# Performance work log

Hardware: AMD Instinct MI355X
Metric: run time of the kernel (lower is better)

## Reference

```python
import jax, jax.numpy as jnp
import numpy as np

B, N, E, IN = 16, 4096, 65536, 128
FILTERS = [256, 256, 128]


def setup_inputs() -> dict:
    key = jax.random.key(0)
    ks = jax.random.split(key, 12)
    inp = {
        "x": jax.random.normal(ks[0], (B, N, IN), dtype=jnp.float32),
        "edge_index": jax.random.randint(ks[1], (B, 2, E), 0, N, dtype=jnp.int32),
        "edge_weight": jax.random.uniform(ks[2], (B, E), dtype=jnp.float32),
        "mask": jax.random.randint(ks[3], (B, N), 0, 2, dtype=jnp.int32),
    }
    dims = [IN] + FILTERS
    for i in range(3):
        inp[f"W{i+1}"] = jax.random.normal(ks[4 + 2 * i], (dims[i], dims[i + 1]), dtype=jnp.float32) / np.sqrt(dims[i]).astype(np.float32)
        inp[f"b{i+1}"] = 0.01 * jax.random.normal(ks[5 + 2 * i], (dims[i + 1],), dtype=jnp.float32)
    return inp


def _gcn_layer(x, ei, ew, valid, W, b):
    # GCNConv(add_self_loops=False, normalize=False):
    #   h = x @ W; out[v] = sum_{(u,v)} ew * h[u]; out += b (valid rows only)
    h = x @ W  # [N, d_out]
    u, v = ei[0], ei[1]
    evalid = valid[u] & valid[v]            # drop edges touching masked-out nodes
    w = jnp.where(evalid, ew, 0.0)
    agg = jnp.zeros_like(h).at[v].add(w[:, None] * h[u])
    return jnp.where(valid[:, None], agg + b, 0.0)


def reference(x, edge_index, edge_weight, mask, W1, b1, W2, b2, W3, b3):
    valid = mask > 0  # [B, N] bool
    out = x
    for W, b in ((W1, b1), (W2, b2), (W3, b3)):
        out = jax.vmap(_gcn_layer, in_axes=(0, 0, 0, 0, None, None))(
            out, edge_index, edge_weight, valid, W, b)
        out = jax.nn.relu(out)  # dropout p=0.0 -> identity
    return out
```

## Files before the change

kernel.cpp:

```cpp
#include <hip/hip_runtime.h>

static constexpr int BATCH = 16;
static constexpr int NNODE = 4096;
static constexpr int NEDGE = 65536;
static constexpr int ROWS  = BATCH * NNODE;
static constexpr int CAP   = 2432;
static constexpr int PM    = BATCH * CAP;

typedef _Float16 half8  __attribute__((ext_vector_type(8)));
typedef _Float16 half4v __attribute__((ext_vector_type(4)));
typedef _Float16 half2v __attribute__((ext_vector_type(2)));
typedef float    f32x4  __attribute__((ext_vector_type(4)));
typedef float    f32x2  __attribute__((ext_vector_type(2)));

#define GP(p) (const __attribute__((address_space(1))) void*)(p)
#define LP(p) (__attribute__((address_space(3))) void*)(p)


__global__ __launch_bounds__(256) void count_kernel(
    const int* __restrict__ ei, const int* __restrict__ mask,
    int* __restrict__ counts)
{
    const int idx = blockIdx.x * 256 + threadIdx.x;
    const int b = idx >> 16;
    const int e = idx & (NEDGE - 1);
    const int* eib = ei + (size_t)b * 2 * NEDGE;
    const int u = eib[e];
    const int v = eib[NEDGE + e];
    const int mrow = b * NNODE;
    if (mask[mrow + u] != 0 && mask[mrow + v] != 0)
        atomicAdd(&counts[mrow + v], 1);
}

__global__ __launch_bounds__(256) void scan_compact_kernel(
    const int* __restrict__ counts, const int* __restrict__ mask,
    int* __restrict__ row_start, int* __restrict__ cursor,
    int* __restrict__ vlist, int* __restrict__ cidx, int* __restrict__ validN)
{
    __shared__ int sums[256];
    const int b = blockIdx.x, t = threadIdx.x;

    const int* mb = mask + b * NNODE;
    for (int i = t; i < CAP; i += 256) vlist[b * CAP + i] = 0;

    int loc[16]; int s = 0;
    #pragma unroll
    for (int i = 0; i < 16; ++i) { loc[i] = (mb[t * 16 + i] != 0); s += loc[i]; }
    sums[t] = s;
    __syncthreads();
    for (int off = 1; off < 256; off <<= 1) {
        int v = (t >= off) ? sums[t - off] : 0;
        __syncthreads();
        sums[t] += v;
        __syncthreads();
    }
    int run = (t == 0) ? 0 : sums[t - 1];
    #pragma unroll
    for (int i = 0; i < 16; ++i) {
        const int n = t * 16 + i;
        if (loc[i]) {
            if (run < CAP) { vlist[b * CAP + run] = n; cidx[b * NNODE + n] = b * CAP + run; }
            ++run;
        } else {
            cidx[b * NNODE + n] = 0;
        }
    }
    if (t == 255) validN[b] = run;
    __syncthreads();

    const int* c = counts + b * NNODE;
    int* rs = row_start + b * (NNODE + 1);
    int* cu = cursor + b * NNODE;

    int local[16]; s = 0;
    #pragma unroll
    for (int i = 0; i < 16; ++i) { local[i] = c[t * 16 + i]; s += local[i]; }
    sums[t] = s;
    __syncthreads();
    for (int off = 1; off < 256; off <<= 1) {
        int v = (t >= off) ? sums[t - off] : 0;
        __syncthreads();
        sums[t] += v;
        __syncthreads();
    }
    run = (t == 0) ? 0 : sums[t - 1];
    #pragma unroll
    for (int i = 0; i < 16; ++i) { rs[t * 16 + i] = run; cu[t * 16 + i] = run; run += local[i]; }
    if (t == 255) rs[NNODE] = run;
}

__global__ __launch_bounds__(256) void fill_kernel(
    const int* __restrict__ ei, const float* __restrict__ ew,
    const int* __restrict__ mask, const int* __restrict__ cidx,
    int* __restrict__ cursor, unsigned int* __restrict__ bkt)
{
    const int idx = blockIdx.x * 256 + threadIdx.x;
    const int b = idx >> 16;
    const int e = idx & (NEDGE - 1);
    const int* eib = ei + (size_t)b * 2 * NEDGE;
    const int u = eib[e];
    const int v = eib[NEDGE + e];
    const int mrow = b * NNODE;
    if (mask[mrow + u] != 0 && mask[mrow + v] != 0) {
        const _Float16 w = (_Float16)ew[(size_t)b * NEDGE + e];
        const unsigned short wb = __builtin_bit_cast(unsigned short, w);
        const unsigned uc = (unsigned)cidx[mrow + u];
        const int pos = atomicAdd(&cursor[mrow + v], 1);
        bkt[(size_t)b * NEDGE + pos] = ((unsigned)wb << 16) | uc;
    }
}


__global__ __launch_bounds__(256) void prep_kernel(
    const float* __restrict__ X, const int* __restrict__ vlist,
    const float* __restrict__ W1, const float* __restrict__ W2,
    const float* __restrict__ W3,
    _Float16* __restrict__ X16c, _Float16* __restrict__ Wt1,
    _Float16* __restrict__ Wt2, _Float16* __restrict__ Wt3)
{
    const int idx = blockIdx.x * 256 + threadIdx.x;
    if (idx < PM * 32) {
        const int row = idx >> 5;
        const int c4  = idx & 31;
        const int b   = row / CAP;
        const int v   = vlist[row];
        const float4 s = *(const float4*)&X[((size_t)b * NNODE + v) * 128 + c4 * 4];
        half4v h = {(_Float16)s.x, (_Float16)s.y, (_Float16)s.z, (_Float16)s.w};
        *(half4v*)&X16c[(size_t)row * 128 + c4 * 4] = h;
    } else {
        const int i = idx - PM * 32;
        if (i < 32768) {
            int k = i >> 8, n = i & 255;
            Wt1[n * 128 + k] = (_Float16)W1[i];
        } else if (i < 98304) {
            int j = i - 32768;
            int k = j >> 8, n = j & 255;
            Wt2[n * 256 + k] = (_Float16)W2[j];
        } else {
            int j = i - 98304;
            int k = j >> 7, n = j & 127;
            Wt3[n * 256 + k] = (_Float16)W3[j];
        }
    }
}

template<int K, int N, bool EPI>
__global__ __launch_bounds__(256, 2) void gemm_full(
    const _Float16* __restrict__ Xc,
    const _Float16* __restrict__ Wt,
    const float* __restrict__ bias,
    _Float16* __restrict__ Hc)
{
    constexpr int NCH  = CAP / 128;
    constexpr int NPAN = K / 32;
    constexpr int NI   = N / 32;
    constexpr int CB   = N / 2;
    constexpr int RST  = CB + 8;
    __shared__ _Float16 A16[NPAN * 128 * 32];

    const int tid  = threadIdx.x;
    const int lane = tid & 63;
    const int wave = tid >> 6;
    const int wr = wave >> 1, wc = wave & 1;
    const int quad = lane >> 4;
    const int l15  = lane & 15;

    const int xcd  = blockIdx.x & 7;
    const int j    = blockIdx.x >> 3;
    const int batch = 2 * xcd + (j >= NCH);
    const int tile  = (j >= NCH) ? j - NCH : j;
    const size_t bm = (size_t)batch * CAP + (size_t)tile * 128;

    const int srow = tid >> 2;
    const int sch  = (tid & 3) * 8;
    #pragma unroll
    for (int pp = 0; pp < NPAN; ++pp)
        #pragma unroll
        for (int rnd = 0; rnd < 2; ++rnd)
            __builtin_amdgcn_global_load_lds(
                GP(Xc + (bm + rnd * 64 + srow) * K + pp * 32 + sch),
                LP(A16 + pp * 4096 + rnd * 2048 + tid * 8), 16, 0, 0);
    __syncthreads();

    f32x4 acc[4][NI];
    #pragma unroll
    for (int mi = 0; mi < 4; ++mi)
        #pragma unroll
        for (int ni = 0; ni < NI; ++ni) acc[mi][ni] = (f32x4)0.0f;

    const _Float16* ap = A16 + (wr * 64 + l15) * 32 + quad * 8;
    const _Float16* wp = Wt + (size_t)(wc * CB + l15) * K + quad * 8;

    #pragma unroll
    for (int pp = 0; pp < NPAN; ++pp) {
        half8 af[4], bf[NI];
        #pragma unroll
        for (int mi = 0; mi < 4; ++mi)
            af[mi] = *(const half8*)(ap + pp * 4096 + mi * 16 * 32);
        #pragma unroll
        for (int ni = 0; ni < NI; ++ni)
            bf[ni] = *(const half8*)(wp + (size_t)ni * 16 * K + pp * 32);
        #pragma unroll
        for (int mi = 0; mi < 4; ++mi)
            #pragma unroll
            for (int ni = 0; ni < NI; ++ni)
                acc[mi][ni] = __builtin_amdgcn_mfma_f32_16x16x32_f16(
                    bf[ni], af[mi], acc[mi][ni], 0, 0, 0);
    }
    __syncthreads();

    _Float16* stg = A16 + wave * 16 * RST;
    const int rr = lane >> 2;
    const int c0 = lane & 3;
    #pragma unroll
    for (int mi = 0; mi < 4; ++mi) {
        #pragma unroll
        for (int ni = 0; ni < NI; ++ni) {
            f32x4 v = acc[mi][ni];
            half4v o;
            if (EPI) {
                const f32x4 bv = *(const f32x4*)&bias[wc * CB + ni * 16 + quad * 4];
                #pragma unroll
                for (int r = 0; r < 4; ++r) o[r] = (_Float16)fmaxf(v[r] + bv[r], 0.0f);
            } else {
                #pragma unroll
                for (int r = 0; r < 4; ++r) o[r] = (_Float16)v[r];
            }
            *(half4v*)&stg[l15 * RST + ni * 16 + quad * 4] = o;
        }
        const size_t grow = bm + wr * 64 + mi * 16 + rr;
        _Float16* hp = &Hc[grow * N + wc * CB];
        #pragma unroll
        for (int c = 0; c < NI / 2; ++c) {
            const int ch = (c0 + 4 * c) * 8;
            half8 v = *(const half8*)&stg[rr * RST + ch];
            *(half8*)(hp + ch) = v;
        }
    }
}

__global__ __launch_bounds__(256, 2) void gemm23_kernel(
    const _Float16* __restrict__ Xc,
    const _Float16* __restrict__ Wt2,
    const _Float16* __restrict__ Wt3,
    const float* __restrict__ b2,
    _Float16* __restrict__ H3)
{
    constexpr int K    = 256;
    constexpr int NPAN = K / 32;
    constexpr int NCH  = CAP / 128;
    __shared__ _Float16 A16[NPAN * 128 * 32];

    const int tid  = threadIdx.x;
    const int lane = tid & 63;
    const int wave = tid >> 6;
    const int wr = wave >> 1, wc = wave & 1;
    const int quad = lane >> 4;
    const int l15  = lane & 15;

    const int xcd  = blockIdx.x & 7;
    const int j    = blockIdx.x >> 3;
    const int batch = 2 * xcd + (j >= NCH);
    const int tile  = (j >= NCH) ? j - NCH : j;
    const size_t bm = (size_t)batch * CAP + (size_t)tile * 128;

    const int srow = tid >> 2;
    const int sch  = (tid & 3) * 8;
    #pragma unroll
    for (int pp = 0; pp < NPAN; ++pp)
        #pragma unroll
        for (int rnd = 0; rnd < 2; ++rnd)
            __builtin_amdgcn_global_load_lds(
                GP(Xc + (bm + rnd * 64 + srow) * K + pp * 32 + sch),
                LP(A16 + pp * 4096 + rnd * 2048 + tid * 8), 16, 0, 0);
    __syncthreads();

    f32x4 acc[4][8];
    #pragma unroll
    for (int mi = 0; mi < 4; ++mi)
        #pragma unroll
        for (int ni = 0; ni < 8; ++ni) acc[mi][ni] = (f32x4)0.0f;

    const _Float16* ap = A16 + (wr * 64 + l15) * 32 + quad * 8;
    const _Float16* wp = Wt2 + (size_t)(wc * 128 + l15) * K + quad * 8;

    #pragma unroll
    for (int pp = 0; pp < NPAN; ++pp) {
        half8 af[4], bf[8];
        #pragma unroll
        for (int mi = 0; mi < 4; ++mi)
            af[mi] = *(const half8*)(ap + pp * 4096 + mi * 16 * 32);
        #pragma unroll
        for (int ni = 0; ni < 8; ++ni)
            bf[ni] = *(const half8*)(wp + (size_t)ni * 16 * K + pp * 32);
        #pragma unroll
        for (int mi = 0; mi < 4; ++mi)
            #pragma unroll
            for (int ni = 0; ni < 8; ++ni)
                acc[mi][ni] = __builtin_amdgcn_mfma_f32_16x16x32_f16(
                    bf[ni], af[mi], acc[mi][ni], 0, 0, 0);
    }
    __syncthreads();

    #pragma unroll
    for (int mi = 0; mi < 4; ++mi) {
        const int row = wr * 64 + mi * 16 + l15;
        #pragma unroll
        for (int ni = 0; ni < 8; ++ni) {
            const int col = wc * 128 + ni * 16 + quad * 4;
            const f32x4 bv = *(const f32x4*)&b2[col];
            f32x4 v = acc[mi][ni];
            half4v o;
            #pragma unroll
            for (int r = 0; r < 4; ++r) o[r] = (_Float16)fmaxf(v[r] + bv[r], 0.0f);
            *(half4v*)&A16[(col >> 5) * 4096 + row * 32 + (col & 31)] = o;
        }
    }
    __syncthreads();

    f32x4 acc2[4][4];
    #pragma unroll
    for (int mi = 0; mi < 4; ++mi)
        #pragma unroll
        for (int ni = 0; ni < 4; ++ni) acc2[mi][ni] = (f32x4)0.0f;

    const _Float16* wp3 = Wt3 + (size_t)(wc * 64 + l15) * K + quad * 8;
    #pragma unroll
    for (int pp = 0; pp < NPAN; ++pp) {
        half8 af[4], bf[4];
        #pragma unroll
        for (int mi = 0; mi < 4; ++mi)
            af[mi] = *(const half8*)(ap + pp * 4096 + mi * 16 * 32);
        #pragma unroll
        for (int ni = 0; ni < 4; ++ni)
            bf[ni] = *(const half8*)(wp3 + (size_t)ni * 16 * K + pp * 32);
        #pragma unroll
        for (int mi = 0; mi < 4; ++mi)
            #pragma unroll
            for (int ni = 0; ni < 4; ++ni)
                acc2[mi][ni] = __builtin_amdgcn_mfma_f32_16x16x32_f16(
                    bf[ni], af[mi], acc2[mi][ni], 0, 0, 0);
    }
    __syncthreads();

    constexpr int RST = 72;
    _Float16* stg = A16 + wave * 16 * RST;
    const int rr = lane >> 2;
    const int c0 = lane & 3;
    #pragma unroll
    for (int mi = 0; mi < 4; ++mi) {
        #pragma unroll
        for (int ni = 0; ni < 4; ++ni) {
            f32x4 v = acc2[mi][ni];
            half4v o;
            #pragma unroll
            for (int r = 0; r < 4; ++r) o[r] = (_Float16)v[r];
            *(half4v*)&stg[l15 * RST + ni * 16 + quad * 4] = o;
        }
        const size_t grow = bm + wr * 64 + mi * 16 + rr;
        _Float16* hp = &H3[grow * 128 + wc * 64];
        #pragma unroll
        for (int c = 0; c < 2; ++c) {
            const int ch = (c0 + 4 * c) * 8;
            half8 v = *(const half8*)&stg[rr * RST + ch];
            *(half8*)(hp + ch) = v;
        }
    }
}


__global__ __launch_bounds__(256) void gather_x(
    const int* __restrict__ row_start, const unsigned int* __restrict__ bkt,
    const _Float16* __restrict__ X,
    const int* __restrict__ vlist, const int* __restrict__ validN,
    _Float16* __restrict__ OUT)
{
    constexpr int NU = CAP / 4;
    const int tid  = threadIdx.x;
    const int lane = tid & 63;
    const int wave = tid >> 6;

    const int xcd  = blockIdx.x & 7;
    const int jj   = blockIdx.x >> 3;
    const int batch = 2 * xcd + (jj >= NU);
    const int unit  = (jj >= NU) ? jj - NU : jj;

    const int j = unit * 4 + wave;
    if (j >= validN[batch]) return;
    const int g = batch * CAP + j;
    const int v = vlist[g];

    const int* rs = row_start + batch * (NNODE + 1);
    const int s = rs[v], e = rs[v + 1];
    const unsigned* bk = bkt + (size_t)batch * NEDGE;
    const _Float16* Hb = X + lane * 2;

    float acc[2] = {};
    for (int i = s; i < e; i += 8) {
        const int cnt = e - i;
        unsigned pk[8];
        #pragma unroll
        for (int t = 0; t < 8; ++t) pk[t] = bk[i + t];
        const unsigned u0 = pk[0] & 0xffffu;
        float wj[8]; const _Float16* hp[8];
        #pragma unroll
        for (int t = 0; t < 8; ++t) {
            const bool ok = (t < cnt);
            const unsigned u = ok ? (pk[t] & 0xffffu) : u0;
            wj[t] = ok ? (float)__builtin_bit_cast(_Float16, (unsigned short)(pk[t] >> 16)) : 0.0f;
            hp[t] = Hb + (size_t)u * 128;
        }
        half2v hv[8];
        #pragma unroll
        for (int t = 0; t < 8; ++t) hv[t] = *(const half2v*)hp[t];
        #pragma unroll
        for (int t = 0; t < 8; ++t)
            #pragma unroll
            for (int c = 0; c < 2; ++c) acc[c] += wj[t] * (float)hv[t][c];
    }
    half2v o = {(_Float16)acc[0], (_Float16)acc[1]};
    *(half2v*)&OUT[(size_t)g * 128 + lane * 2] = o;
}

__global__ __launch_bounds__(256) void gather_agg(
    const int* __restrict__ row_start, const unsigned int* __restrict__ bkt,
    const _Float16* __restrict__ H,
    const int* __restrict__ vlist, const int* __restrict__ validN,
    _Float16* __restrict__ OUT)
{
    constexpr int NU = CAP / 4;
    const int tid  = threadIdx.x;
    const int lane = tid & 63;
    const int wave = tid >> 6;

    const int xcd  = blockIdx.x & 7;
    const int jj   = blockIdx.x >> 3;
    const int batch = 2 * xcd + (jj >= NU);
    const int unit  = (jj >= NU) ? jj - NU : jj;

    const int j = unit * 4 + wave;
    if (j >= validN[batch]) return;
    const int g = batch * CAP + j;
    const int v = vlist[g];

    const int* rs = row_start + batch * (NNODE + 1);
    const int s = rs[v], e = rs[v + 1];
    const unsigned* bk = bkt + (size_t)batch * NEDGE;
    const _Float16* Hb = H + lane * 4;

    float acc[4] = {};
    for (int i = s; i < e; i += 8) {
        const int cnt = e - i;
        unsigned pk[8];
        #pragma unroll
        for (int t = 0; t < 8; ++t) pk[t] = bk[i + t];
        const unsigned u0 = pk[0] & 0xffffu;
        float wj[8]; const _Float16* hp[8];
        #pragma unroll
        for (int t = 0; t < 8; ++t) {
            const bool ok = (t < cnt);
            const unsigned u = ok ? (pk[t] & 0xffffu) : u0;
            wj[t] = ok ? (float)__builtin_bit_cast(_Float16, (unsigned short)(pk[t] >> 16)) : 0.0f;
            hp[t] = Hb + (size_t)u * 256;
        }
        half4v hv[8];
        #pragma unroll
        for (int t = 0; t < 8; ++t) hv[t] = *(const half4v*)hp[t];
        #pragma unroll
        for (int t = 0; t < 8; ++t)
            #pragma unroll
            for (int c = 0; c < 4; ++c) acc[c] += wj[t] * (float)hv[t][c];
    }
    half4v o;
    #pragma unroll
    for (int c = 0; c < 4; ++c) o[c] = (_Float16)acc[c];
    *(half4v*)&OUT[(size_t)g * 256 + lane * 4] = o;
}

__global__ __launch_bounds__(256) void gather_final(
    const int* __restrict__ row_start, const unsigned int* __restrict__ bkt,
    const _Float16* __restrict__ H,
    const int* __restrict__ mask, const float* __restrict__ bias,
    float* __restrict__ OUT)
{
    constexpr int NU = NNODE / 4;
    const int tid  = threadIdx.x;
    const int lane = tid & 63;
    const int wave = tid >> 6;

    const int xcd  = blockIdx.x & 7;
    const int jj   = blockIdx.x >> 3;
    const int batch = 2 * xcd + (jj >= NU);
    const int unit  = (jj >= NU) ? jj - NU : jj;

    const int n = unit * 4 + wave;
    const int mrow = batch * NNODE + n;

    float acc[2] = {};
    if (mask[mrow] != 0) {
        const int* rs = row_start + batch * (NNODE + 1);
        const int s = rs[n], e = rs[n + 1];
        const unsigned* bk = bkt + (size_t)batch * NEDGE;
        const _Float16* Hb = H + lane * 2;

        for (int i = s; i < e; i += 8) {
            const int cnt = e - i;
            unsigned pk[8];
            #pragma unroll
            for (int t = 0; t < 8; ++t) pk[t] = bk[i + t];
            const unsigned u0 = pk[0] & 0xffffu;
            float wj[8]; const _Float16* hp[8];
            #pragma unroll
            for (int t = 0; t < 8; ++t) {
                const bool ok = (t < cnt);
                const unsigned u = ok ? (pk[t] & 0xffffu) : u0;
                wj[t] = ok ? (float)__builtin_bit_cast(_Float16, (unsigned short)(pk[t] >> 16)) : 0.0f;
                hp[t] = Hb + (size_t)u * 128;
            }
            half2v hv[8];
            #pragma unroll
            for (int t = 0; t < 8; ++t) hv[t] = *(const half2v*)hp[t];
            #pragma unroll
            for (int t = 0; t < 8; ++t)
                #pragma unroll
                for (int c = 0; c < 2; ++c) acc[c] += wj[t] * (float)hv[t][c];
        }
        #pragma unroll
        for (int c = 0; c < 2; ++c)
            acc[c] = fmaxf(acc[c] + bias[lane * 2 + c], 0.0f);
    }
    f32x2 o = {acc[0], acc[1]};
    *(f32x2*)&OUT[(size_t)mrow * 128 + lane * 2] = o;
}

extern "C" void kernel_launch(void* const* d_in, const int* in_sizes, int n_in,
                              void* d_out, int out_size, void* d_ws, size_t ws_size,
                              hipStream_t stream) {
    const float* x    = (const float*)d_in[0];
    const int*   ei   = (const int*)  d_in[1];
    const float* ew   = (const float*)d_in[2];
    const int*   mask = (const int*)  d_in[3];
    const float* W1   = (const float*)d_in[4];
    const float* b1   = (const float*)d_in[5];
    const float* W2   = (const float*)d_in[6];
    const float* b2   = (const float*)d_in[7];
    const float* W3   = (const float*)d_in[8];
    const float* b3   = (const float*)d_in[9];
    float* out = (float*)d_out;

    char* ws = (char*)d_ws;
    _Float16* X16c = (_Float16*)(ws);
    _Float16* AggX = (_Float16*)(ws + (10u << 20));
    _Float16* H3c  = AggX;
    _Float16* Ac   = (_Float16*)(ws + (20u << 20));
    _Float16* AggA = (_Float16*)(ws + (40u << 20));
    unsigned int* bkt = (unsigned int*)(ws + (60u << 20));
    _Float16* Wt1  = (_Float16*)(ws + (64u << 20));
    _Float16* Wt2  = Wt1 + 128 * 256;
    _Float16* Wt3  = Wt2 + 256 * 256;
    int* counts    = (int*)(Wt3 + 256 * 128);
    int* row_start = counts + ROWS;
    int* cursor    = row_start + BATCH * (NNODE + 1);
    int* cidx      = cursor + ROWS;
    int* vlist     = cidx + ROWS;
    int* validN    = vlist + PM;

    const dim3 blk(256);
    const int edgeBlocks = BATCH * NEDGE / 256;

    hipMemsetAsync(counts, 0, (size_t)ROWS * sizeof(int), stream);
    count_kernel<<<edgeBlocks, blk, 0, stream>>>(ei, mask, counts);
    scan_compact_kernel<<<BATCH, blk, 0, stream>>>(counts, mask, row_start, cursor,
                                                   vlist, cidx, validN);
    fill_kernel<<<edgeBlocks, blk, 0, stream>>>(ei, ew, mask, cidx, cursor, bkt);

    const int prepBlocks = (PM * 32 + 131072) / 256;
    prep_kernel<<<prepBlocks, blk, 0, stream>>>(x, vlist, W1, W2, W3,
                                                X16c, Wt1, Wt2, Wt3);

    const int gemmBlocks = PM / 128;
    const int midBlocks  = PM / 4;
    const int finBlocks  = ROWS / 4;

    gather_x<<<midBlocks, blk, 0, stream>>>(row_start, bkt, X16c, vlist, validN, AggX);
    gemm_full<128, 256, true><<<gemmBlocks, blk, 0, stream>>>(AggX, Wt1, b1, Ac);

    gather_agg<<<midBlocks, blk, 0, stream>>>(row_start, bkt, Ac, vlist, validN, AggA);
    gemm23_kernel<<<gemmBlocks, blk, 0, stream>>>(AggA, Wt2, Wt3, b2, H3c);

    gather_final<<<finBlocks, blk, 0, stream>>>(row_start, bkt, H3c, mask, b3, out);
}
```

Baseline: 242.6 us.

## Split scan into parallel blocks, fuse fill with prep, halve GEMM row tiles

The scan/compact kernel now runs mask compaction and count scan in separate blocks (2*BATCH blocks) instead of serially within one block. The edge-fill and X/weight prep kernels are merged into one launch, which removes a launch and lets both phases overlap. Both GEMM kernels move from 128-row to 64-row tiles, with each wave owning a column slice, and launch bounds rise to 3 blocks per CU. This doubles the grid and raises occupancy, at the cost of loading each weight column once per 64 rows instead of per 128.

```diff
diff --git a/kernel.cpp b/kernel.cpp
--- a/kernel.cpp
+++ b/kernel.cpp
@@ -38,130 +38,131 @@
     int* __restrict__ vlist, int* __restrict__ cidx, int* __restrict__ validN)
 {
     __shared__ int sums[256];
-    const int b = blockIdx.x, t = threadIdx.x;
-
-    const int* mb = mask + b * NNODE;
-    for (int i = t; i < CAP; i += 256) vlist[b * CAP + i] = 0;
-
-    int loc[16]; int s = 0;
-    #pragma unroll
-    for (int i = 0; i < 16; ++i) { loc[i] = (mb[t * 16 + i] != 0); s += loc[i]; }
-    sums[t] = s;
-    __syncthreads();
-    for (int off = 1; off < 256; off <<= 1) {
-        int v = (t >= off) ? sums[t - off] : 0;
+    const int t = threadIdx.x;
+
+    if (blockIdx.x < BATCH) {
+        const int b = blockIdx.x;
+        const int* c = counts + b * NNODE;
+        int* rs = row_start + b * (NNODE + 1);
+        int* cu = cursor + b * NNODE;
+
+        int local[16]; int s = 0;
+        #pragma unroll
+        for (int i = 0; i < 16; ++i) { local[i] = c[t * 16 + i]; s += local[i]; }
+        sums[t] = s;
         __syncthreads();
-        sums[t] += v;
+        for (int off = 1; off < 256; off <<= 1) {
+            int v = (t >= off) ? sums[t - off] : 0;
+            __syncthreads();
+            sums[t] += v;
+            __syncthreads();
+        }
+        int run = (t == 0) ? 0 : sums[t - 1];
+        #pragma unroll
+        for (int i = 0; i < 16; ++i) { rs[t * 16 + i] = run; cu[t * 16 + i] = run; run += local[i]; }
+        if (t == 255) rs[NNODE] = run;
+    } else {
+        const int b = blockIdx.x - BATCH;
+        const int* mb = mask + b * NNODE;
+        for (int i = t; i < CAP; i += 256) vlist[b * CAP + i] = 0;
+
+        int loc[16]; int s = 0;
+        #pragma unroll
+        for (int i = 0; i < 16; ++i) { loc[i] = (mb[t * 16 + i] != 0); s += loc[i]; }
+        sums[t] = s;
         __syncthreads();
-    }
-    int run = (t == 0) ? 0 : sums[t - 1];
-    #pragma unroll
-    for (int i = 0; i < 16; ++i) {
-        const int n = t * 16 + i;
-        if (loc[i]) {
-            if (run < CAP) { vlist[b * CAP + run] = n; cidx[b * NNODE + n] = b * CAP + run; }
-            ++run;
-        } else {
-            cidx[b * NNODE + n] = 0;
-        }
-    }
-    if (t == 255) validN[b] = run;
-    __syncthreads();
-
-    const int* c = counts + b * NNODE;
-    int* rs = row_start + b * (NNODE + 1);
-    int* cu = cursor + b * NNODE;
-
-    int local[16]; s = 0;
-    #pragma unroll
-    for (int i = 0; i < 16; ++i) { local[i] = c[t * 16 + i]; s += local[i]; }
-    sums[t] = s;
-    __syncthreads();
-    for (int off = 1; off < 256; off <<= 1) {
-        int v = (t >= off) ? sums[t - off] : 0;
-        __syncthreads();
-        sums[t] += v;
-        __syncthreads();
-    }
-    run = (t == 0) ? 0 : sums[t - 1];
-    #pragma unroll
-    for (int i = 0; i < 16; ++i) { rs[t * 16 + i] = run; cu[t * 16 + i] = run; run += local[i]; }
-    if (t == 255) rs[NNODE] = run;
-}
-
-__global__ __launch_bounds__(256) void fill_kernel(
+        for (int off = 1; off < 256; off <<= 1) {
+            int v = (t >= off) ? sums[t - off] : 0;
+            __syncthreads();
+            sums[t] += v;
+            __syncthreads();
+        }
+        int run = (t == 0) ? 0 : sums[t - 1];
+        #pragma unroll
+        for (int i = 0; i < 16; ++i) {
+            const int n = t * 16 + i;
+            if (loc[i]) {
+                if (run < CAP) { vlist[b * CAP + run] = n; cidx[b * NNODE + n] = b * CAP + run; }
+                ++run;
+            } else {
+                cidx[b * NNODE + n] = 0;
+            }
+        }
+        if (t == 255) validN[b] = run;
+    }
+}
+
+__global__ __launch_bounds__(256) void fill_prep_kernel(
     const int* __restrict__ ei, const float* __restrict__ ew,
     const int* __restrict__ mask, const int* __restrict__ cidx,
-    int* __restrict__ cursor, unsigned int* __restrict__ bkt)
-{
-    const int idx = blockIdx.x * 256 + threadIdx.x;
-    const int b = idx >> 16;
-    const int e = idx & (NEDGE - 1);
-    const int* eib = ei + (size_t)b * 2 * NEDGE;
-    const int u = eib[e];
-    const int v = eib[NEDGE + e];
-    const int mrow = b * NNODE;
-    if (mask[mrow + u] != 0 && mask[mrow + v] != 0) {
-        const _Float16 w = (_Float16)ew[(size_t)b * NEDGE + e];
-        const unsigned short wb = __builtin_bit_cast(unsigned short, w);
-        const unsigned uc = (unsigned)cidx[mrow + u];
-        const int pos = atomicAdd(&cursor[mrow + v], 1);
-        bkt[(size_t)b * NEDGE + pos] = ((unsigned)wb << 16) | uc;
-    }
-}
-
-
-__global__ __launch_bounds__(256) void prep_kernel(
+    int* __restrict__ cursor, unsigned int* __restrict__ bkt,
     const float* __restrict__ X, const int* __restrict__ vlist,
     const float* __restrict__ W1, const float* __restrict__ W2,
     const float* __restrict__ W3,
     _Float16* __restrict__ X16c, _Float16* __restrict__ Wt1,
     _Float16* __restrict__ Wt2, _Float16* __restrict__ Wt3)
 {
-    const int idx = blockIdx.x * 256 + threadIdx.x;
-    if (idx < PM * 32) {
-        const int row = idx >> 5;
-        const int c4  = idx & 31;
-        const int b   = row / CAP;
-        const int v   = vlist[row];
-        const float4 s = *(const float4*)&X[((size_t)b * NNODE + v) * 128 + c4 * 4];
-        half4v h = {(_Float16)s.x, (_Float16)s.y, (_Float16)s.z, (_Float16)s.w};
-        *(half4v*)&X16c[(size_t)row * 128 + c4 * 4] = h;
+    const int blk = blockIdx.x;
+    if (blk < 4096) {
+        const int idx = blk * 256 + threadIdx.x;
+        const int b = idx >> 16;
+        const int e = idx & (NEDGE - 1);
+        const int* eib = ei + (size_t)b * 2 * NEDGE;
+        const int u = eib[e];
+        const int v = eib[NEDGE + e];
+        const int mrow = b * NNODE;
+        if (mask[mrow + u] != 0 && mask[mrow + v] != 0) {
+            const _Float16 w = (_Float16)ew[(size_t)b * NEDGE + e];
+            const unsigned short wb = __builtin_bit_cast(unsigned short, w);
+            const unsigned uc = (unsigned)cidx[mrow + u];
+            const int pos = atomicAdd(&cursor[mrow + v], 1);
+            bkt[(size_t)b * NEDGE + pos] = ((unsigned)wb << 16) | uc;
+        }
     } else {
-        const int i = idx - PM * 32;
-        if (i < 32768) {
-            int k = i >> 8, n = i & 255;
-            Wt1[n * 128 + k] = (_Float16)W1[i];
-        } else if (i < 98304) {
-            int j = i - 32768;
-            int k = j >> 8, n = j & 255;
-            Wt2[n * 256 + k] = (_Float16)W2[j];
+        const int idx = (blk - 4096) * 256 + threadIdx.x;
+        if (idx < PM * 32) {
+            const int row = idx >> 5;
+            const int c4  = idx & 31;
+            const int b   = row / CAP;
+            const int v   = vlist[row];
+            const float4 s = *(const float4*)&X[((size_t)b * NNODE + v) * 128 + c4 * 4];
+            half4v h = {(_Float16)s.x, (_Float16)s.y, (_Float16)s.z, (_Float16)s.w};
+            *(half4v*)&X16c[(size_t)row * 128 + c4 * 4] = h;
         } else {
-            int j = i - 98304;
-            int k = j >> 7, n = j & 127;
-            Wt3[n * 256 + k] = (_Float16)W3[j];
+            const int i = idx - PM * 32;
+            if (i < 32768) {
+                int k = i >> 8, n = i & 255;
+                Wt1[n * 128 + k] = (_Float16)W1[i];
+            } else if (i < 98304) {
+                int j = i - 32768;
+                int k = j >> 8, n = j & 255;
+                Wt2[n * 256 + k] = (_Float16)W2[j];
+            } else {
+                int j = i - 98304;
+                int k = j >> 7, n = j & 127;
+                Wt3[n * 256 + k] = (_Float16)W3[j];
+            }
         }
     }
 }
 
 template<int K, int N, bool EPI>
-__global__ __launch_bounds__(256, 2) void gemm_full(
+__global__ __launch_bounds__(256, 3) void gemm_full(
     const _Float16* __restrict__ Xc,
     const _Float16* __restrict__ Wt,
     const float* __restrict__ bias,
     _Float16* __restrict__ Hc)
 {
-    constexpr int NCH  = CAP / 128;
+    constexpr int NCH  = CAP / 64;
     constexpr int NPAN = K / 32;
-    constexpr int NI   = N / 32;
-    constexpr int CB   = N / 2;
-    constexpr int RST  = CB + 8;
-    __shared__ _Float16 A16[NPAN * 128 * 32];
+    constexpr int NW   = N / 4;
+    constexpr int NI   = NW / 16;
+    constexpr int RST  = NW + 8;
+    __shared__ _Float16 A16[NPAN * 64 * 32];
 
     const int tid  = threadIdx.x;
     const int lane = tid & 63;
     const int wave = tid >> 6;
-    const int wr = wave >> 1, wc = wave & 1;
     const int quad = lane >> 4;
     const int l15  = lane & 15;
 
@@ -169,17 +170,15 @@
     const int j    = blockIdx.x >> 3;
     const int batch = 2 * xcd + (j >= NCH);
     const int tile  = (j >= NCH) ? j - NCH : j;
-    const size_t bm = (size_t)batch * CAP + (size_t)tile * 128;
+    const size_t bm = (size_t)batch * CAP + (size_t)tile * 64;
 
     const int srow = tid >> 2;
     const int sch  = (tid & 3) * 8;
     #pragma unroll
     for (int pp = 0; pp < NPAN; ++pp)
-        #pragma unroll
-        for (int rnd = 0; rnd < 2; ++rnd)
-            __builtin_amdgcn_global_load_lds(
-                GP(Xc + (bm + rnd * 64 + srow) * K + pp * 32 + sch),
-                LP(A16 + pp * 4096 + rnd * 2048 + tid * 8), 16, 0, 0);
+        __builtin_amdgcn_global_load_lds(
+            GP(Xc + (bm + srow) * K + pp * 32 + sch),
+            LP(A16 + pp * 2048 + tid * 8), 16, 0, 0);
     __syncthreads();
 
     f32x4 acc[4][NI];
@@ -188,15 +187,15 @@
         #pragma unroll
         for (int ni = 0; ni < NI; ++ni) acc[mi][ni] = (f32x4)0.0f;
 
-    const _Float16* ap = A16 + (wr * 64 + l15) * 32 + quad * 8;
-    const _Float16* wp = Wt + (size_t)(wc * CB + l15) * K + quad * 8;
+    const _Float16* ap = A16 + l15 * 32 + quad * 8;
+    const _Float16* wp = Wt + (size_t)(wave * NW + l15) * K + quad * 8;
 
     #pragma unroll
     for (int pp = 0; pp < NPAN; ++pp) {
         half8 af[4], bf[NI];
         #pragma unroll
         for (int mi = 0; mi < 4; ++mi)
-            af[mi] = *(const half8*)(ap + pp * 4096 + mi * 16 * 32);
+            af[mi] = *(const half8*)(ap + pp * 2048 + mi * 16 * 32);
         #pragma unroll
         for (int ni = 0; ni < NI; ++ni)
             bf[ni] = *(const half8*)(wp + (size_t)ni * 16 * K + pp * 32);
@@ -219,7 +218,7 @@
             f32x4 v = acc[mi][ni];
             half4v o;
             if (EPI) {
-                const f32x4 bv = *(const f32x4*)&bias[wc * CB + ni * 16 + quad * 4];
+                const f32x4 bv = *(const f32x4*)&bias[wave * NW + ni * 16 + quad * 4];
                 #pragma unroll
                 for (int r = 0; r < 4; ++r) o[r] = (_Float16)fmaxf(v[r] + bv[r], 0.0f);
             } else {
@@ -228,8 +227,8 @@
             }
             *(half4v*)&stg[l15 * RST + ni * 16 + quad * 4] = o;
         }
-        const size_t grow = bm + wr * 64 + mi * 16 + rr;
-        _Float16* hp = &Hc[grow * N + wc * CB];
+        const size_t grow = bm + mi * 16 + rr;
+        _Float16* hp = &Hc[grow * N + wave * NW];
         #pragma unroll
         for (int c = 0; c < NI / 2; ++c) {
             const int ch = (c0 + 4 * c) * 8;
@@ -239,7 +238,7 @@
     }
 }
 
-__global__ __launch_bounds__(256, 2) void gemm23_kernel(
+__global__ __launch_bounds__(256, 3) void gemm23_kernel(
     const _Float16* __restrict__ Xc,
     const _Float16* __restrict__ Wt2,
     const _Float16* __restrict__ Wt3,
@@ -248,13 +247,12 @@
 {
     constexpr int K    = 256;
     constexpr int NPAN = K / 32;
-    constexpr int NCH  = CAP / 128;
-    __shared__ _Float16 A16[NPAN * 128 * 32];
+    constexpr int NCH  = CAP / 64;
+    __shared__ _Float16 A16[NPAN * 64 * 32];
 
     const int tid  = threadIdx.x;
     const int lane = tid & 63;
     const int wave = tid >> 6;
-    const int wr = wave >> 1, wc = wave & 1;
     const int quad = lane >> 4;
     const int l15  = lane & 15;
 
@@ -262,41 +260,39 @@
     const int j    = blockIdx.x >> 3;
     const int batch = 2 * xcd + (j >= NCH);
     const int tile  = (j >= NCH) ? j - NCH : j;
-    const size_t bm = (size_t)batch * CAP + (size_t)tile * 128;
+    const size_t bm = (size_t)batch * CAP + (size_t)tile * 64;
 
     const int srow = tid >> 2;
     const int sch  = (tid & 3) * 8;
     #pragma unroll
     for (int pp = 0; pp < NPAN; ++pp)
-        #pragma unroll
-        for (int rnd = 0; rnd < 2; ++rnd)
-            __builtin_amdgcn_global_load_lds(
-                GP(Xc + (bm + rnd * 64 + srow) * K + pp * 32 + sch),
-                LP(A16 + pp * 4096 + rnd * 2048 + tid * 8), 16, 0, 0);
+        __builtin_amdgcn_global_load_lds(
+            GP(Xc + (bm + srow) * K + pp * 32 + sch),
+            LP(A16 + pp * 2048 + tid * 8), 16, 0, 0);
     __syncthreads();
 
-    f32x4 acc[4][8];
+    f32x4 acc[4][4];
     #pragma unroll
     for (int mi = 0; mi < 4; ++mi)
         #pragma unroll
-        for (int ni = 0; ni < 8; ++ni) acc[mi][ni] = (f32x4)0.0f;
-
-    const _Float16* ap = A16 + (wr * 64 + l15) * 32 + quad * 8;
-    const _Float16* wp = Wt2 + (size_t)(wc * 128 + l15) * K + quad * 8;
+        for (int ni = 0; ni < 4; ++ni) acc[mi][ni] = (f32x4)0.0f;
+
+    const _Float16* ap = A16 + l15 * 32 + quad * 8;
+    const _Float16* wp = Wt2 + (size_t)(wave * 64 + l15) * K + quad * 8;
 
     #pragma unroll
     for (int pp = 0; pp < NPAN; ++pp) {
-        half8 af[4], bf[8];
+        half8 af[4], bf[4];
         #pragma unroll
         for (int mi = 0; mi < 4; ++mi)
-            af[mi] = *(const half8*)(ap + pp * 4096 + mi * 16 * 32);
-        #pragma unroll
-        for (int ni = 0; ni < 8; ++ni)
+            af[mi] = *(const half8*)(ap + pp * 2048 + mi * 16 * 32);
+        #pragma unroll
+        for (int ni = 0; ni < 4; ++ni)
             bf[ni] = *(const half8*)(wp + (size_t)ni * 16 * K + pp * 32);
         #pragma unroll
         for (int mi = 0; mi < 4; ++mi)
             #pragma unroll
-            for (int ni = 0; ni < 8; ++ni)
+            for (int ni = 0; ni < 4; ++ni)
                 acc[mi][ni] = __builtin_amdgcn_mfma_f32_16x16x32_f16(
                     bf[ni], af[mi], acc[mi][ni], 0, 0, 0);
     }
@@ -304,64 +300,63 @@
 
     #pragma unroll
     for (int mi = 0; mi < 4; ++mi) {
-        const int row = wr * 64 + mi * 16 + l15;
-        #pragma unroll
-        for (int ni = 0; ni < 8; ++ni) {
-            const int col = wc * 128 + ni * 16 + quad * 4;
+        const int row = mi * 16 + l15;
+        #pragma unroll
+        for (int ni = 0; ni < 4; ++ni) {
+            const int col = wave * 64 + ni * 16 + quad * 4;
             const f32x4 bv = *(const f32x4*)&b2[col];
             f32x4 v = acc[mi][ni];
             half4v o;
             #pragma unroll
             for (int r = 0; r < 4; ++r) o[r] = (_Float16)fmaxf(v[r] + bv[r], 0.0f);
-            *(half4v*)&A16[(col >> 5) * 4096 + row * 32 + (col & 31)] = o;
+            *(half4v*)&A16[(col >> 5) * 2048 + row * 32 + (col & 31)] = o;
         }
     }
     __syncthreads();
 
-    f32x4 acc2[4][4];
+    f32x4 acc2[4][2];
     #pragma unroll
     for (int mi = 0; mi < 4; ++mi)
         #pragma unroll
-        for (int ni = 0; ni < 4; ++ni) acc2[mi][ni] = (f32x4)0.0f;
-
-    const _Float16* wp3 = Wt3 + (size_t)(wc * 64 + l15) * K + quad * 8;
+        for (int ni = 0; ni < 2; ++ni) acc2[mi][ni] = (f32x4)0.0f;
+
+    const _Float16* wp3 = Wt3 + (size_t)(wave * 32 + l15) * K + quad * 8;
     #pragma unroll
     for (int pp = 0; pp < NPAN; ++pp) {
-        half8 af[4], bf[4];
+        half8 af[4], bf[2];
         #pragma unroll
         for (int mi = 0; mi < 4; ++mi)
-            af[mi] = *(const half8*)(ap + pp * 4096 + mi * 16 * 32);
-        #pragma unroll
-        for (int ni = 0; ni < 4; ++ni)
+            af[mi] = *(const half8*)(ap + pp * 2048 + mi * 16 * 32);
+        #pragma unroll
+        for (int ni = 0; ni < 2; ++ni)
             bf[ni] = *(const half8*)(wp3 + (size_t)ni * 16 * K + pp * 32);
         #pragma unroll
         for (int mi = 0; mi < 4; ++mi)
             #pragma unroll
-            for (int ni = 0; ni < 4; ++ni)
+            for (int ni = 0; ni < 2; ++ni)
                 acc2[mi][ni] = __builtin_amdgcn_mfma_f32_16x16x32_f16(
                     bf[ni], af[mi], acc2[mi][ni], 0, 0, 0);
     }
     __syncthreads();
 
-    constexpr int RST = 72;
+    constexpr int RST = 40;
     _Float16* stg = A16 + wave * 16 * RST;
     const int rr = lane >> 2;
     const int c0 = lane & 3;
     #pragma unroll
     for (int mi = 0; mi < 4; ++mi) {
         #pragma unroll
-        for (int ni = 0; ni < 4; ++ni) {
+        for (int ni = 0; ni < 2; ++ni) {
             f32x4 v = acc2[mi][ni];
             half4v o;
             #pragma unroll
             for (int r = 0; r < 4; ++r) o[r] = (_Float16)v[r];
             *(half4v*)&stg[l15 * RST + ni * 16 + quad * 4] = o;
         }
-        const size_t grow = bm + wr * 64 + mi * 16 + rr;
-        _Float16* hp = &H3[grow * 128 + wc * 64];
-        #pragma unroll
-        for (int c = 0; c < 2; ++c) {
-            const int ch = (c0 + 4 * c) * 8;
+        const size_t grow = bm + mi * 16 + rr;
+        _Float16* hp = &H3[grow * 128 + wave * 32];
+        {
+            const int ch = c0 * 8;
             half8 v = *(const half8*)&stg[rr * RST + ch];
             *(half8*)(hp + ch) = v;
         }
@@ -570,15 +565,14 @@
 
     hipMemsetAsync(counts, 0, (size_t)ROWS * sizeof(int), stream);
     count_kernel<<<edgeBlocks, blk, 0, stream>>>(ei, mask, counts);
-    scan_compact_kernel<<<BATCH, blk, 0, stream>>>(counts, mask, row_start, cursor,
-                                                   vlist, cidx, validN);
-    fill_kernel<<<edgeBlocks, blk, 0, stream>>>(ei, ew, mask, cidx, cursor, bkt);
-
+    scan_compact_kernel<<<2 * BATCH, blk, 0, stream>>>(counts, mask, row_start, cursor,
+                                                       vlist, cidx, validN);
     const int prepBlocks = (PM * 32 + 131072) / 256;
-    prep_kernel<<<prepBlocks, blk, 0, stream>>>(x, vlist, W1, W2, W3,
-                                                X16c, Wt1, Wt2, Wt3);
-
-    const int gemmBlocks = PM / 128;
+    fill_prep_kernel<<<edgeBlocks + prepBlocks, blk, 0, stream>>>(
+        ei, ew, mask, cidx, cursor, bkt, x, vlist, W1, W2, W3,
+        X16c, Wt1, Wt2, Wt3);
+
+    const int gemmBlocks = PM / 64;
     const int midBlocks  = PM / 4;
     const int finBlocks  = ROWS / 4;
 
```

Result: faster. 228.0 us (-6.0%).
